# Performance work log

Hardware: AMD Instinct MI355X
Metric: run time of the kernel (lower is better)

Reference implementation:

```python
import jax, jax.numpy as jnp
import numpy as np

H = 1024
BATCH, T = 16, 2048

def setup_inputs() -> dict:
    key = jax.random.key(0)
    k1, k2, k3, k4 = jax.random.split(key, 4)
    scale = 1.0 / (H ** 0.5)
    return {
        "u_sequence": jax.random.normal(k1, (BATCH, T, 1), dtype=jnp.float32),
        "A": jax.random.normal(k2, (H, H), dtype=jnp.float32) * scale,
        "B": jax.random.normal(k3, (H, 1), dtype=jnp.float32) * scale,
        "C": jax.random.normal(k4, (1, H), dtype=jnp.float32) * scale,
        "D": jnp.zeros((1,), dtype=jnp.float32),
    }

def reference(u_sequence, A, B, C, D):
    # u_sequence: [Bt, T, 1]
    u = u_sequence[..., 0]            # [Bt, T]
    b_vec = B[:, 0]                   # [H]

    def step(h, u_t):
        # h: [Bt, H], u_t: [Bt]
        h_new = h @ A.T + u_t[:, None] * b_vec[None, :]
        return h_new, h_new

    h0 = jnp.zeros((u.shape[0], H), dtype=u.dtype)
    _, h_stack = jax.lax.scan(step, h0, u.T)   # h_stack: [T, Bt, H]
    h_stack = jnp.swapaxes(h_stack, 0, 1)      # [Bt, T, H]
    y = jnp.einsum("bth,h->bt", h_stack, C[0]) + u * D[0]
    return y[..., None]                         # [Bt, T, 1]
```

## Files before the change

kernel.cpp:

```cpp
#include <hip/hip_runtime.h>

#define HDIM 1024
#define TLEN 2048
#define NBATCH 16

typedef short bf16x8 __attribute__((ext_vector_type(8)));
typedef float floatx4 __attribute__((ext_vector_type(4)));
typedef unsigned short ushort_t;

__device__ __forceinline__ ushort_t f2bf(float x) {
  unsigned u = __float_as_uint(x);
  unsigned r = (u + 0x7FFFu + ((u >> 16) & 1u)) >> 16;
  return (ushort_t)r;
}
__device__ __forceinline__ float bf2f(ushort_t h) {
  return __uint_as_float(((unsigned)h) << 16);
}

#define LSTR 40
#define TSTR 71

__global__ __launch_bounds__(256) void prep(const float* __restrict__ A,
    const float* __restrict__ Bv, const float* __restrict__ Cv,
    ushort_t* __restrict__ Ah, ushort_t* __restrict__ Am, ushort_t* __restrict__ Al,
    ushort_t* __restrict__ ATh, ushort_t* __restrict__ ATm, ushort_t* __restrict__ ATl,
    float* __restrict__ Vc, float* __restrict__ U) {
  __shared__ ushort_t Lt[3 * 64 * TSTR];
  const int tid = threadIdx.x;
  if (blockIdx.x >= 256) {
    int i = (blockIdx.x - 256) * 256 + tid;
    if (i < HDIM) Vc[i] = Bv[i];
    else U[i - HDIM] = Cv[i - HDIM];
    return;
  }
  const int row0 = (blockIdx.x >> 4) * 64, col0 = (blockIdx.x & 15) * 64;
  const int r = tid >> 2, q = tid & 3;
  ushort_t hs[16], ms[16], ls[16];
#pragma unroll
  for (int c4 = 0; c4 < 4; ++c4) {
    float4 a = *(const float4*)&A[(row0 + r) * HDIM + col0 + q * 16 + c4 * 4];
    float av[4] = {a.x, a.y, a.z, a.w};
#pragma unroll
    for (int i = 0; i < 4; ++i) {
      float z = av[i];
      ushort_t h = f2bf(z); float r1 = z - bf2f(h);
      ushort_t mq = f2bf(r1); float r2 = r1 - bf2f(mq);
      ushort_t lq = f2bf(r2);
      hs[c4 * 4 + i] = h; ms[c4 * 4 + i] = mq; ls[c4 * 4 + i] = lq;
    }
  }
  size_t go = (size_t)(row0 + r) * HDIM + col0 + q * 16;
  *(uint4*)&Ah[go] = ((uint4*)hs)[0]; *(uint4*)&Ah[go + 8] = ((uint4*)hs)[1];
  *(uint4*)&Am[go] = ((uint4*)ms)[0]; *(uint4*)&Am[go + 8] = ((uint4*)ms)[1];
  *(uint4*)&Al[go] = ((uint4*)ls)[0]; *(uint4*)&Al[go + 8] = ((uint4*)ls)[1];
#pragma unroll
  for (int i = 0; i < 16; ++i) {
    int c = q * 16 + i;
    Lt[0 * 64 * TSTR + r * TSTR + c] = hs[i];
    Lt[1 * 64 * TSTR + r * TSTR + c] = ms[i];
    Lt[2 * 64 * TSTR + r * TSTR + c] = ls[i];
  }
  __syncthreads();
  const int c = tid >> 2, q2 = tid & 3;
  ushort_t* dsts[3] = {ATh, ATm, ATl};
#pragma unroll
  for (int s = 0; s < 3; ++s) {
    ushort_t tmp[16];
#pragma unroll
    for (int rr = 0; rr < 16; ++rr) tmp[rr] = Lt[s * 64 * TSTR + (q2 * 16 + rr) * TSTR + c];
    size_t gt = (size_t)(col0 + c) * HDIM + row0 + q2 * 16;
    *(uint4*)&dsts[s][gt] = ((uint4*)tmp)[0];
    *(uint4*)&dsts[s][gt + 8] = ((uint4*)tmp)[1];
  }
}

template <int MODE, int NC, bool SIX, bool WRITEL>
__global__ __launch_bounds__(256) void sq_mfma(
    const ushort_t* __restrict__ Xh, const ushort_t* __restrict__ Xm,
    const ushort_t* __restrict__ Xl,
    const ushort_t* __restrict__ XTh, const ushort_t* __restrict__ XTm,
    const ushort_t* __restrict__ XTl,
    ushort_t* __restrict__ Zh, ushort_t* __restrict__ Zm, ushort_t* __restrict__ Zl,
    ushort_t* __restrict__ ZTh, ushort_t* __restrict__ ZTm, ushort_t* __restrict__ ZTl,
    const float* __restrict__ Af, const float* __restrict__ Bvf,
    float* __restrict__ VU) {
  __shared__ ushort_t sm[6 * 64 * LSTR];
  const int tid = threadIdx.x;

  if (blockIdx.x >= 256) {
    const int tb = blockIdx.x - 256;
    const int wv = tb * 4 + (tid >> 6);
    const int lane = tid & 63;
    if (MODE == 0) {
      float acc = 0.f;
      for (int k = lane; k < HDIM; k += 64) acc += Af[(size_t)wv * HDIM + k] * Bvf[k];
      for (int off = 32; off; off >>= 1) acc += __shfl_down(acc, off);
      if (lane == 0) VU[HDIM + wv] = acc;
    } else {
      const ushort_t* Ph = (MODE == 1) ? Xh : XTh;
      const ushort_t* Pm = (MODE == 1) ? Xm : XTm;
      float acc[NC];
#pragma unroll
      for (int n = 0; n < NC; ++n) acc[n] = 0.f;
      for (int k = lane; k < HDIM; k += 64) {
        float a = bf2f(Ph[(size_t)wv * HDIM + k]) + bf2f(Pm[(size_t)wv * HDIM + k]);
#pragma unroll
        for (int n = 0; n < NC; ++n) acc[n] += a * VU[(size_t)n * HDIM + k];
      }
#pragma unroll
      for (int n = 0; n < NC; ++n) {
        float s = acc[n];
        for (int off = 32; off; off >>= 1) s += __shfl_down(s, off);
        if (lane == 0) VU[(size_t)(NC + n) * HDIM + wv] = s;
      }
    }
    return;
  }

  const int bb = blockIdx.x;
  const int xcd = bb & 7, slot = bb >> 3;
  const int tr = 4 * (xcd >> 1) + (slot >> 3);
  const int tc = 8 * (xcd & 1) + (slot & 7);
  const int row0 = tr * 64, col0 = tc * 64;

  const int AH = 0, AM = 64 * LSTR, AL = 2 * 64 * LSTR;
  const int BH = 3 * 64 * LSTR, BM = 4 * 64 * LSTR, BL = 5 * 64 * LSTR;
  const int w = tid >> 6, l = tid & 63, li = l & 15, quad = l >> 4;
  const int sr = tid >> 2, sq4 = tid & 3;

  floatx4 acc0 = {0.f, 0.f, 0.f, 0.f}, acc1 = acc0, acc2 = acc0, acc3 = acc0;

  const int aoff = (w * 16 + li) * LSTR + quad * 8;
  const int b0o = (0 * 16 + li) * LSTR + quad * 8;
  const int b1o = (1 * 16 + li) * LSTR + quad * 8;
  const int b2o = (2 * 16 + li) * LSTR + quad * 8;
  const int b3o = (3 * 16 + li) * LSTR + quad * 8;
  const int soff = sr * LSTR + sq4 * 8;
  const size_t gA = (size_t)(row0 + sr) * HDIM + sq4 * 8;
  const size_t gB = (size_t)(col0 + sr) * HDIM + sq4 * 8;

  uint4 pa0 = *(const uint4*)&Xh[gA], pa1 = *(const uint4*)&Xm[gA];
  uint4 pb0 = *(const uint4*)&XTh[gB], pb1 = *(const uint4*)&XTm[gB];
  uint4 pa2, pb2;
  if (SIX) { pa2 = *(const uint4*)&Xl[gA]; pb2 = *(const uint4*)&XTl[gB]; }

  for (int k0 = 0; k0 < HDIM; k0 += 32) {
    __syncthreads();
    *(uint4*)&sm[AH + soff] = pa0;
    *(uint4*)&sm[AM + soff] = pa1;
    *(uint4*)&sm[BH + soff] = pb0;
    *(uint4*)&sm[BM + soff] = pb1;
    if (SIX) {
      *(uint4*)&sm[AL + soff] = pa2;
      *(uint4*)&sm[BL + soff] = pb2;
    }
    __syncthreads();
    if (k0 + 32 < HDIM) {
      pa0 = *(const uint4*)&Xh[gA + k0 + 32];
      pa1 = *(const uint4*)&Xm[gA + k0 + 32];
      pb0 = *(const uint4*)&XTh[gB + k0 + 32];
      pb1 = *(const uint4*)&XTm[gB + k0 + 32];
      if (SIX) {
        pa2 = *(const uint4*)&Xl[gA + k0 + 32];
        pb2 = *(const uint4*)&XTl[gB + k0 + 32];
      }
    }
    bf16x8 ah = *(const bf16x8*)&sm[AH + aoff];
    bf16x8 am = *(const bf16x8*)&sm[AM + aoff];
    bf16x8 al;
    if (SIX) al = *(const bf16x8*)&sm[AL + aoff];
    {
      bf16x8 bh = *(const bf16x8*)&sm[BH + b0o];
      bf16x8 bm = *(const bf16x8*)&sm[BM + b0o];
      acc0 = __builtin_amdgcn_mfma_f32_16x16x32_bf16(ah, bh, acc0, 0, 0, 0);
      acc0 = __builtin_amdgcn_mfma_f32_16x16x32_bf16(ah, bm, acc0, 0, 0, 0);
      acc0 = __builtin_amdgcn_mfma_f32_16x16x32_bf16(am, bh, acc0, 0, 0, 0);
      acc0 = __builtin_amdgcn_mfma_f32_16x16x32_bf16(am, bm, acc0, 0, 0, 0);
      if (SIX) {
        bf16x8 bl = *(const bf16x8*)&sm[BL + b0o];
        acc0 = __builtin_amdgcn_mfma_f32_16x16x32_bf16(ah, bl, acc0, 0, 0, 0);
        acc0 = __builtin_amdgcn_mfma_f32_16x16x32_bf16(al, bh, acc0, 0, 0, 0);
      }
    }
    {
      bf16x8 bh = *(const bf16x8*)&sm[BH + b1o];
      bf16x8 bm = *(const bf16x8*)&sm[BM + b1o];
      acc1 = __builtin_amdgcn_mfma_f32_16x16x32_bf16(ah, bh, acc1, 0, 0, 0);
      acc1 = __builtin_amdgcn_mfma_f32_16x16x32_bf16(ah, bm, acc1, 0, 0, 0);
      acc1 = __builtin_amdgcn_mfma_f32_16x16x32_bf16(am, bh, acc1, 0, 0, 0);
      acc1 = __builtin_amdgcn_mfma_f32_16x16x32_bf16(am, bm, acc1, 0, 0, 0);
      if (SIX) {
        bf16x8 bl = *(const bf16x8*)&sm[BL + b1o];
        acc1 = __builtin_amdgcn_mfma_f32_16x16x32_bf16(ah, bl, acc1, 0, 0, 0);
        acc1 = __builtin_amdgcn_mfma_f32_16x16x32_bf16(al, bh, acc1, 0, 0, 0);
      }
    }
    {
      bf16x8 bh = *(const bf16x8*)&sm[BH + b2o];
      bf16x8 bm = *(const bf16x8*)&sm[BM + b2o];
      acc2 = __builtin_amdgcn_mfma_f32_16x16x32_bf16(ah, bh, acc2, 0, 0, 0);
      acc2 = __builtin_amdgcn_mfma_f32_16x16x32_bf16(ah, bm, acc2, 0, 0, 0);
      acc2 = __builtin_amdgcn_mfma_f32_16x16x32_bf16(am, bh, acc2, 0, 0, 0);
      acc2 = __builtin_amdgcn_mfma_f32_16x16x32_bf16(am, bm, acc2, 0, 0, 0);
      if (SIX) {
        bf16x8 bl = *(const bf16x8*)&sm[BL + b2o];
        acc2 = __builtin_amdgcn_mfma_f32_16x16x32_bf16(ah, bl, acc2, 0, 0, 0);
        acc2 = __builtin_amdgcn_mfma_f32_16x16x32_bf16(al, bh, acc2, 0, 0, 0);
      }
    }
    {
      bf16x8 bh = *(const bf16x8*)&sm[BH + b3o];
      bf16x8 bm = *(const bf16x8*)&sm[BM + b3o];
      acc3 = __builtin_amdgcn_mfma_f32_16x16x32_bf16(ah, bh, acc3, 0, 0, 0);
      acc3 = __builtin_amdgcn_mfma_f32_16x16x32_bf16(ah, bm, acc3, 0, 0, 0);
      acc3 = __builtin_amdgcn_mfma_f32_16x16x32_bf16(am, bh, acc3, 0, 0, 0);
      acc3 = __builtin_amdgcn_mfma_f32_16x16x32_bf16(am, bm, acc3, 0, 0, 0);
      if (SIX) {
        bf16x8 bl = *(const bf16x8*)&sm[BL + b3o];
        acc3 = __builtin_amdgcn_mfma_f32_16x16x32_bf16(ah, bl, acc3, 0, 0, 0);
        acc3 = __builtin_amdgcn_mfma_f32_16x16x32_bf16(al, bh, acc3, 0, 0, 0);
      }
    }
  }

  __syncthreads();
  floatx4 accs[4] = {acc0, acc1, acc2, acc3};
#pragma unroll
  for (int j = 0; j < 4; ++j) {
#pragma unroll
    for (int e = 0; e < 4; ++e) {
      float z = accs[j][e];
      int rl = w * 16 + quad * 4 + e;
      int cl = j * 16 + li;
      size_t go = (size_t)(row0 + rl) * HDIM + col0 + cl;
      ushort_t h = f2bf(z); float r1 = z - bf2f(h);
      ushort_t mq = f2bf(r1);
      Zh[go] = h; Zm[go] = mq;
      sm[0 * 64 * TSTR + rl * TSTR + cl] = h;
      sm[1 * 64 * TSTR + rl * TSTR + cl] = mq;
      if (WRITEL) {
        ushort_t lq = f2bf(r1 - bf2f(mq));
        Zl[go] = lq;
        sm[2 * 64 * TSTR + rl * TSTR + cl] = lq;
      }
    }
  }
  __syncthreads();
  const int c = tid >> 2, q2 = tid & 3;
  ushort_t* dsts[3] = {ZTh, ZTm, ZTl};
  const int npass = WRITEL ? 3 : 2;
#pragma unroll
  for (int s = 0; s < 3; ++s) {
    if (s >= npass) break;
    ushort_t tmp[16];
#pragma unroll
    for (int rr = 0; rr < 16; ++rr) tmp[rr] = sm[s * 64 * TSTR + (q2 * 16 + rr) * TSTR + c];
    size_t gt = (size_t)(col0 + c) * HDIM + row0 + q2 * 16;
    *(uint4*)&dsts[s][gt] = ((uint4*)tmp)[0];
    *(uint4*)&dsts[s][gt + 8] = ((uint4*)tmp)[1];
  }
}

__global__ __launch_bounds__(256) void utail8(const ushort_t* __restrict__ PTh,
                                              const ushort_t* __restrict__ PTm,
                                              float* __restrict__ U, int dstbase) {
  const int wv = blockIdx.x * 4 + (threadIdx.x >> 6);
  const int lane = threadIdx.x & 63;
  float acc[8];
#pragma unroll
  for (int m = 0; m < 8; ++m) acc[m] = 0.f;
  const float* Usrc = U + (size_t)(dstbase - 8) * HDIM;
  for (int k = lane; k < HDIM; k += 64) {
    float a = bf2f(PTh[(size_t)wv * HDIM + k]) + bf2f(PTm[(size_t)wv * HDIM + k]);
#pragma unroll
    for (int m = 0; m < 8; ++m) acc[m] += a * Usrc[(size_t)m * HDIM + k];
  }
#pragma unroll
  for (int m = 0; m < 8; ++m) {
    float s = acc[m];
    for (int off = 32; off; off >>= 1) s += __shfl_down(s, off);
    if (lane == 0) U[(size_t)(dstbase + m) * HDIM + wv] = s;
  }
}

__global__ __launch_bounds__(256) void wavedotK(const float* __restrict__ U,
                                                const float* __restrict__ Vc,
                                                float* __restrict__ Km) {
  int wv = (blockIdx.x * blockDim.x + threadIdx.x) >> 6;
  int lane = threadIdx.x & 63;
  if (wv >= 32 * 64) return;
  int mr = wv >> 6;
  int nc = wv & 63;
  float s = 0.f;
  for (int k = lane; k < HDIM; k += 64) s += U[mr * HDIM + k] * Vc[nc * HDIM + k];
  for (int off = 32; off; off >>= 1) s += __shfl_down(s, off);
  if (lane == 0) Km[wv] = s;
}

__global__ __launch_bounds__(256) void convk2(const float* __restrict__ u,
                                              const float* __restrict__ Km,
                                              const float* __restrict__ Dv,
                                              float* __restrict__ y) {
  __shared__ float ks[256];
  __shared__ float us[512];
  const int tt = threadIdx.x;
  const int t0 = blockIdx.x * 256;
  const int b = blockIdx.y;
  const float* ub = u + (size_t)b * TLEN;
  const int t = t0 + tt;
  float s = Dv[0] * ub[t];
  for (int mc = 0; mc <= t0; mc += 256) {
    __syncthreads();
    ks[tt] = Km[mc + tt];
    int w0 = t0 - mc - 255;
    int g0 = w0 + tt;
    us[tt] = (g0 >= 0) ? ub[g0] : 0.f;
    int g1 = w0 + 256 + tt;
    us[256 + tt] = (g1 < TLEN) ? ub[g1] : 0.f;
    __syncthreads();
    if (mc < t0) {
#pragma unroll 4
      for (int r = 0; r < 256; r += 4) {
        float4 kv = *(const float4*)&ks[r];
        s += kv.x * us[tt - r + 255];
        s += kv.y * us[tt - r + 254];
        s += kv.z * us[tt - r + 253];
        s += kv.w * us[tt - r + 252];
      }
    } else {
      for (int r = 0; r <= tt; ++r) s += ks[r] * us[tt - r + 255];
    }
  }
  y[(size_t)b * TLEN + t] = s;
}

extern "C" void kernel_launch(void* const* d_in, const int* in_sizes, int n_in,
                              void* d_out, int out_size, void* d_ws, size_t ws_size,
                              hipStream_t stream) {
  const float* u  = (const float*)d_in[0];
  const float* A  = (const float*)d_in[1];
  const float* Bv = (const float*)d_in[2];
  const float* Cv = (const float*)d_in[3];
  const float* Dv = (const float*)d_in[4];
  float* out = (float*)d_out;

  char* wsb = (char*)d_ws;
  size_t off = 0;
  ushort_t* S[2][6];
  for (int s = 0; s < 2; ++s)
    for (int a = 0; a < 6; ++a) { S[s][a] = (ushort_t*)(wsb + off); off += (size_t)2 << 20; }
  float* Vc = (float*)(wsb + off); off += 64 * HDIM * 4;
  float* U  = (float*)(wsb + off); off += 32 * HDIM * 4;
  float* Km = (float*)(wsb + off); off += TLEN * 4;

  const dim3 gsq(512);

#define SQ(MODE, NC, SIX, WRL, IN, OUT, VU)                                    \
  sq_mfma<MODE, NC, SIX, WRL><<<gsq, 256, 0, stream>>>(                        \
      S[IN][0], S[IN][1], S[IN][2], S[IN][3], S[IN][4], S[IN][5],              \
      S[OUT][0], S[OUT][1], S[OUT][2], S[OUT][3], S[OUT][4], S[OUT][5],        \
      A, Bv, VU)

  prep<<<dim3(264), 256, 0, stream>>>(A, Bv, Cv,
      S[0][0], S[0][1], S[0][2], S[0][3], S[0][4], S[0][5], Vc, U);

  SQ(0, 1,  true,  true,  0, 1, Vc);
  SQ(1, 2,  true,  true,  1, 0, Vc);
  SQ(1, 4,  true,  true,  0, 1, Vc);
  SQ(1, 8,  true,  false, 1, 0, Vc);
  SQ(1, 16, false, false, 0, 1, Vc);
  SQ(1, 32, false, false, 1, 0, Vc);
  SQ(2, 1,  false, false, 0, 1, U);
  SQ(2, 2,  false, false, 1, 0, U);
  SQ(2, 4,  false, false, 0, 1, U);
#undef SQ

  utail8<<<dim3(256), 256, 0, stream>>>(S[1][3], S[1][4], U, 8);
  utail8<<<dim3(256), 256, 0, stream>>>(S[1][3], S[1][4], U, 16);
  utail8<<<dim3(256), 256, 0, stream>>>(S[1][3], S[1][4], U, 24);

  wavedotK<<<dim3(512), 256, 0, stream>>>(U, Vc, Km);
  convk2<<<dim3(TLEN / 256, NBATCH), 256, 0, stream>>>(u, Km, Dv, out);
}
```

Measured before the change: 332.1 us.

## Stream GEMM tiles into double-buffered LDS with direct global_load_lds

```diff
diff --git a/kernel.cpp b/kernel.cpp
--- a/kernel.cpp
+++ b/kernel.cpp
@@ -17,7 +17,12 @@
   return __uint_as_float(((unsigned)h) << 16);
 }
 
-#define LSTR 40
+typedef __attribute__((address_space(1))) void gvoid_t;
+typedef __attribute__((address_space(3))) void lvoid_t;
+__device__ __forceinline__ void gload16(const ushort_t* g, ushort_t* l) {
+  __builtin_amdgcn_global_load_lds((gvoid_t*)g, (lvoid_t*)l, 16, 0, 0);
+}
+
 #define TSTR 71
 
 __global__ __launch_bounds__(256) void prep(const float* __restrict__ A,
@@ -84,7 +89,12 @@
     ushort_t* __restrict__ ZTh, ushort_t* __restrict__ ZTm, ushort_t* __restrict__ ZTl,
     const float* __restrict__ Af, const float* __restrict__ Bvf,
     float* __restrict__ VU) {
-  __shared__ ushort_t sm[6 * 64 * LSTR];
+  constexpr int NARR = SIX ? 6 : 4;
+  constexpr int SLAB = 64 * 32;
+  constexpr int BUFSTR = NARR * SLAB;
+  constexpr int BBASE = (SIX ? 3 : 2) * SLAB;
+  constexpr int LDS_ELEMS = 2 * BUFSTR;
+  __shared__ __align__(16) ushort_t sm[LDS_ELEMS];
   const int tid = threadIdx.x;
 
   if (blockIdx.x >= 256) {
@@ -123,107 +133,114 @@
   const int tc = 8 * (xcd & 1) + (slot & 7);
   const int row0 = tr * 64, col0 = tc * 64;
 
-  const int AH = 0, AM = 64 * LSTR, AL = 2 * 64 * LSTR;
-  const int BH = 3 * 64 * LSTR, BM = 4 * 64 * LSTR, BL = 5 * 64 * LSTR;
   const int w = tid >> 6, l = tid & 63, li = l & 15, quad = l >> 4;
   const int sr = tid >> 2, sq4 = tid & 3;
 
   floatx4 acc0 = {0.f, 0.f, 0.f, 0.f}, acc1 = acc0, acc2 = acc0, acc3 = acc0;
 
-  const int aoff = (w * 16 + li) * LSTR + quad * 8;
-  const int b0o = (0 * 16 + li) * LSTR + quad * 8;
-  const int b1o = (1 * 16 + li) * LSTR + quad * 8;
-  const int b2o = (2 * 16 + li) * LSTR + quad * 8;
-  const int b3o = (3 * 16 + li) * LSTR + quad * 8;
-  const int soff = sr * LSTR + sq4 * 8;
-  const size_t gA = (size_t)(row0 + sr) * HDIM + sq4 * 8;
-  const size_t gB = (size_t)(col0 + sr) * HDIM + sq4 * 8;
-
-  uint4 pa0 = *(const uint4*)&Xh[gA], pa1 = *(const uint4*)&Xm[gA];
-  uint4 pb0 = *(const uint4*)&XTh[gB], pb1 = *(const uint4*)&XTm[gB];
-  uint4 pa2, pb2;
-  if (SIX) { pa2 = *(const uint4*)&Xl[gA]; pb2 = *(const uint4*)&XTl[gB]; }
-
+  const int aoff = (w * 16 + li) * 32 + quad * 8;
+  const int b0o = (0 * 16 + li) * 32 + quad * 8;
+  const int b1o = (1 * 16 + li) * 32 + quad * 8;
+  const int b2o = (2 * 16 + li) * 32 + quad * 8;
+  const int b3o = (3 * 16 + li) * 32 + quad * 8;
+
+  const ushort_t* gAh = Xh + (size_t)(row0 + sr) * HDIM + sq4 * 8;
+  const ushort_t* gAm = Xm + (size_t)(row0 + sr) * HDIM + sq4 * 8;
+  const ushort_t* gAl = Xl + (size_t)(row0 + sr) * HDIM + sq4 * 8;
+  const ushort_t* gBh = XTh + (size_t)(col0 + sr) * HDIM + sq4 * 8;
+  const ushort_t* gBm = XTm + (size_t)(col0 + sr) * HDIM + sq4 * 8;
+  const ushort_t* gBl = XTl + (size_t)(col0 + sr) * HDIM + sq4 * 8;
+
+  ushort_t* lwb = &sm[w * 512];
+
+  {
+    ushort_t* lb = lwb;
+    gload16(gAh, lb);
+    gload16(gAm, lb + SLAB);
+    gload16(gBh, lb + BBASE);
+    gload16(gBm, lb + BBASE + SLAB);
+    if (SIX) {
+      gload16(gAl, lb + 2 * SLAB);
+      gload16(gBl, lb + BBASE + 2 * SLAB);
+    }
+  }
+  __syncthreads();
+
+  int cur = 0;
   for (int k0 = 0; k0 < HDIM; k0 += 32) {
-    __syncthreads();
-    *(uint4*)&sm[AH + soff] = pa0;
-    *(uint4*)&sm[AM + soff] = pa1;
-    *(uint4*)&sm[BH + soff] = pb0;
-    *(uint4*)&sm[BM + soff] = pb1;
-    if (SIX) {
-      *(uint4*)&sm[AL + soff] = pa2;
-      *(uint4*)&sm[BL + soff] = pb2;
-    }
-    __syncthreads();
     if (k0 + 32 < HDIM) {
-      pa0 = *(const uint4*)&Xh[gA + k0 + 32];
-      pa1 = *(const uint4*)&Xm[gA + k0 + 32];
-      pb0 = *(const uint4*)&XTh[gB + k0 + 32];
-      pb1 = *(const uint4*)&XTm[gB + k0 + 32];
+      ushort_t* lb = lwb + (cur ^ 1) * BUFSTR;
+      const int kn = k0 + 32;
+      gload16(gAh + kn, lb);
+      gload16(gAm + kn, lb + SLAB);
+      gload16(gBh + kn, lb + BBASE);
+      gload16(gBm + kn, lb + BBASE + SLAB);
       if (SIX) {
-        pa2 = *(const uint4*)&Xl[gA + k0 + 32];
-        pb2 = *(const uint4*)&XTl[gB + k0 + 32];
-      }
-    }
-    bf16x8 ah = *(const bf16x8*)&sm[AH + aoff];
-    bf16x8 am = *(const bf16x8*)&sm[AM + aoff];
+        gload16(gAl + kn, lb + 2 * SLAB);
+        gload16(gBl + kn, lb + BBASE + 2 * SLAB);
+      }
+    }
+    const int cb = cur * BUFSTR;
+    bf16x8 ah = *(const bf16x8*)&sm[cb + aoff];
+    bf16x8 am = *(const bf16x8*)&sm[cb + SLAB + aoff];
     bf16x8 al;
-    if (SIX) al = *(const bf16x8*)&sm[AL + aoff];
+    if (SIX) al = *(const bf16x8*)&sm[cb + 2 * SLAB + aoff];
     {
-      bf16x8 bh = *(const bf16x8*)&sm[BH + b0o];
-      bf16x8 bm = *(const bf16x8*)&sm[BM + b0o];
+      bf16x8 bh = *(const bf16x8*)&sm[cb + BBASE + b0o];
+      bf16x8 bm = *(const bf16x8*)&sm[cb + BBASE + SLAB + b0o];
       acc0 = __builtin_amdgcn_mfma_f32_16x16x32_bf16(ah, bh, acc0, 0, 0, 0);
       acc0 = __builtin_amdgcn_mfma_f32_16x16x32_bf16(ah, bm, acc0, 0, 0, 0);
       acc0 = __builtin_amdgcn_mfma_f32_16x16x32_bf16(am, bh, acc0, 0, 0, 0);
       acc0 = __builtin_amdgcn_mfma_f32_16x16x32_bf16(am, bm, acc0, 0, 0, 0);
       if (SIX) {
-        bf16x8 bl = *(const bf16x8*)&sm[BL + b0o];
+        bf16x8 bl = *(const bf16x8*)&sm[cb + BBASE + 2 * SLAB + b0o];
         acc0 = __builtin_amdgcn_mfma_f32_16x16x32_bf16(ah, bl, acc0, 0, 0, 0);
         acc0 = __builtin_amdgcn_mfma_f32_16x16x32_bf16(al, bh, acc0, 0, 0, 0);
       }
     }
     {
-      bf16x8 bh = *(const bf16x8*)&sm[BH + b1o];
-      bf16x8 bm = *(const bf16x8*)&sm[BM + b1o];
+      bf16x8 bh = *(const bf16x8*)&sm[cb + BBASE + b1o];
+      bf16x8 bm = *(const bf16x8*)&sm[cb + BBASE + SLAB + b1o];
       acc1 = __builtin_amdgcn_mfma_f32_16x16x32_bf16(ah, bh, acc1, 0, 0, 0);
       acc1 = __builtin_amdgcn_mfma_f32_16x16x32_bf16(ah, bm, acc1, 0, 0, 0);
       acc1 = __builtin_amdgcn_mfma_f32_16x16x32_bf16(am, bh, acc1, 0, 0, 0);
       acc1 = __builtin_amdgcn_mfma_f32_16x16x32_bf16(am, bm, acc1, 0, 0, 0);
       if (SIX) {
-        bf16x8 bl = *(const bf16x8*)&sm[BL + b1o];
+        bf16x8 bl = *(const bf16x8*)&sm[cb + BBASE + 2 * SLAB + b1o];
         acc1 = __builtin_amdgcn_mfma_f32_16x16x32_bf16(ah, bl, acc1, 0, 0, 0);
         acc1 = __builtin_amdgcn_mfma_f32_16x16x32_bf16(al, bh, acc1, 0, 0, 0);
       }
     }
     {
-      bf16x8 bh = *(const bf16x8*)&sm[BH + b2o];
-      bf16x8 bm = *(const bf16x8*)&sm[BM + b2o];
+      bf16x8 bh = *(const bf16x8*)&sm[cb + BBASE + b2o];
+      bf16x8 bm = *(const bf16x8*)&sm[cb + BBASE + SLAB + b2o];
       acc2 = __builtin_amdgcn_mfma_f32_16x16x32_bf16(ah, bh, acc2, 0, 0, 0);
       acc2 = __builtin_amdgcn_mfma_f32_16x16x32_bf16(ah, bm, acc2, 0, 0, 0);
       acc2 = __builtin_amdgcn_mfma_f32_16x16x32_bf16(am, bh, acc2, 0, 0, 0);
       acc2 = __builtin_amdgcn_mfma_f32_16x16x32_bf16(am, bm, acc2, 0, 0, 0);
       if (SIX) {
-        bf16x8 bl = *(const bf16x8*)&sm[BL + b2o];
+        bf16x8 bl = *(const bf16x8*)&sm[cb + BBASE + 2 * SLAB + b2o];
         acc2 = __builtin_amdgcn_mfma_f32_16x16x32_bf16(ah, bl, acc2, 0, 0, 0);
         acc2 = __builtin_amdgcn_mfma_f32_16x16x32_bf16(al, bh, acc2, 0, 0, 0);
       }
     }
     {
-      bf16x8 bh = *(const bf16x8*)&sm[BH + b3o];
-      bf16x8 bm = *(const bf16x8*)&sm[BM + b3o];
+      bf16x8 bh = *(const bf16x8*)&sm[cb + BBASE + b3o];
+      bf16x8 bm = *(const bf16x8*)&sm[cb + BBASE + SLAB + b3o];
       acc3 = __builtin_amdgcn_mfma_f32_16x16x32_bf16(ah, bh, acc3, 0, 0, 0);
       acc3 = __builtin_amdgcn_mfma_f32_16x16x32_bf16(ah, bm, acc3, 0, 0, 0);
       acc3 = __builtin_amdgcn_mfma_f32_16x16x32_bf16(am, bh, acc3, 0, 0, 0);
       acc3 = __builtin_amdgcn_mfma_f32_16x16x32_bf16(am, bm, acc3, 0, 0, 0);
       if (SIX) {
-        bf16x8 bl = *(const bf16x8*)&sm[BL + b3o];
+        bf16x8 bl = *(const bf16x8*)&sm[cb + BBASE + 2 * SLAB + b3o];
         acc3 = __builtin_amdgcn_mfma_f32_16x16x32_bf16(ah, bl, acc3, 0, 0, 0);
         acc3 = __builtin_amdgcn_mfma_f32_16x16x32_bf16(al, bh, acc3, 0, 0, 0);
       }
     }
-  }
-
-  __syncthreads();
+    __syncthreads();
+    cur ^= 1;
+  }
+
   floatx4 accs[4] = {acc0, acc1, acc2, acc3};
 #pragma unroll
   for (int j = 0; j < 4; ++j) {
```

Result: faster. 315.3 us (-5.1%).
